# Optimization experiments

Hardware: AMD Instinct MI355X
Metric: run time of the kernel (lower is better)

Reference implementation:

```python
import jax, jax.numpy as jnp
import numpy as np

N_AGENTS = 8
STATE_DIM = 256
EMBED_DIM = 32
BATCH = 65536


def setup_inputs() -> dict:
    key = jax.random.key(0)
    ks = jax.random.split(key, 12)
    s = 1.0 / np.sqrt(STATE_DIM)
    se = 1.0 / np.sqrt(EMBED_DIM)
    return {
        "agent_qs": jax.random.normal(ks[0], (BATCH, N_AGENTS), dtype=jnp.float32),
        "states": jax.random.normal(ks[1], (BATCH, STATE_DIM), dtype=jnp.float32),
        # hyper_w_1: Linear(state_dim, embed_dim * n_agents)
        "w1_W": jax.random.uniform(ks[2], (STATE_DIM, EMBED_DIM * N_AGENTS), jnp.float32, -s, s),
        "w1_b": jax.random.uniform(ks[3], (EMBED_DIM * N_AGENTS,), jnp.float32, -s, s),
        # hyper_w_final: Linear(state_dim, embed_dim)
        "wf_W": jax.random.uniform(ks[4], (STATE_DIM, EMBED_DIM), jnp.float32, -s, s),
        "wf_b": jax.random.uniform(ks[5], (EMBED_DIM,), jnp.float32, -s, s),
        # hyper_b_1: Linear(state_dim, embed_dim)
        "b1_W": jax.random.uniform(ks[6], (STATE_DIM, EMBED_DIM), jnp.float32, -s, s),
        "b1_b": jax.random.uniform(ks[7], (EMBED_DIM,), jnp.float32, -s, s),
        # V: Linear(state_dim, embed_dim) -> ReLU -> Linear(embed_dim, 1)
        "v1_W": jax.random.uniform(ks[8], (STATE_DIM, EMBED_DIM), jnp.float32, -s, s),
        "v1_b": jax.random.uniform(ks[9], (EMBED_DIM,), jnp.float32, -s, s),
        "v2_W": jax.random.uniform(ks[10], (EMBED_DIM, 1), jnp.float32, -se, se),
        "v2_b": jax.random.uniform(ks[11], (1,), jnp.float32, -se, se),
    }


def reference(agent_qs, states, w1_W, w1_b, wf_W, wf_b, b1_W, b1_b, v1_W, v1_b, v2_W, v2_b):
    B = agent_qs.shape[0]
    # hypernet weights (abs for monotonicity)
    w1 = jnp.abs(states @ w1_W + w1_b).reshape(B, N_AGENTS, EMBED_DIM)   # [B, A, E]
    w_final = jnp.abs(states @ wf_W + wf_b)                               # [B, E]
    b1 = states @ b1_W + b1_b                                             # [B, E]
    # hidden = elu(agent_qs^T w1 + b1): [B,1,A] @ [B,A,E] -> [B,E]
    hidden = jax.nn.elu(jnp.einsum("ba,bae->be", agent_qs, w1) + b1)
    # mixed = hidden @ w_final: [B,1,E] @ [B,E,1] -> [B,1]
    mixed = jnp.sum(hidden * w_final, axis=-1, keepdims=True)             # [B, 1]
    # state value V(s)
    state_value = jax.nn.relu(states @ v1_W + v1_b) @ v2_W + v2_b         # [B, 1]
    return mixed + state_value
```

## Files before the change

### kernel.cpp

```cpp
#include <hip/hip_runtime.h>
#include <math.h>


#define NTILES 22
#define KCHUNKS 8
#define CHUNK_I4 1408

typedef __attribute__((ext_vector_type(8))) short short8;
typedef __attribute__((ext_vector_type(4))) float float4v;

__device__ __forceinline__ unsigned short f2b(float f) {
    unsigned int u = __float_as_uint(f);
    u = u + 0x7fffu + ((u >> 16) & 1u);
    return (unsigned short)(u >> 16);
}

__device__ __forceinline__ void gl2lds16(const unsigned short* g, unsigned short* l) {
    __builtin_amdgcn_global_load_lds(
        (const __attribute__((address_space(1))) unsigned int*)g,
        (__attribute__((address_space(3))) unsigned int*)l,
        16, 0, 0);
}

__global__ void repack_b(const float* __restrict__ w1_W,
                         const float* __restrict__ wf_W,
                         const float* __restrict__ b1_W,
                         const float* __restrict__ v1_W,
                         unsigned short* __restrict__ brep) {
    int idx = blockIdx.x * 256 + threadIdx.x;
    int lane = idx & 63;
    int tt   = idx >> 6;
    int t    = tt % 22;
    int kc   = tt / 22;
    int kbase = kc * 32 + (lane >> 4) * 8;
    int n = t * 16 + (lane & 15);
    short8 frag;
#pragma unroll
    for (int j = 0; j < 8; ++j) {
        int k = kbase + j;
        float val;
        if (n < 256)      val = w1_W[k * 256 + n];
        else if (n < 288) val = wf_W[k * 32 + (n - 256)];
        else if (n < 320) val = b1_W[k * 32 + (n - 288)];
        else              val = v1_W[k * 32 + (n - 320)];
        frag[j] = (short)f2b(val);
    }
    *(short8*)(&brep[idx * 8]) = frag;
}

__global__ void __launch_bounds__(256, 2)
qmix_main(const float* __restrict__ agent_qs,
          const float* __restrict__ states,
          const unsigned short* __restrict__ brep,
          const float* __restrict__ w1_b,
          const float* __restrict__ wf_b,
          const float* __restrict__ b1_b,
          const float* __restrict__ v1_b,
          const float* __restrict__ v2_W,
          const float* __restrict__ v2_b,
          float* __restrict__ out) {
    __shared__ __align__(16) unsigned short wlds[2][NTILES * 64 * 8];

    const int tid  = threadIdx.x;
    const int wave = tid >> 6, lane = tid & 63;
    const int quad = lane >> 4, l16 = lane & 15;
    const int r0 = blockIdx.x * 128 + wave * 32 + l16;
    const float* srow0 = states + (size_t)r0 * 256;
    const float* srow1 = srow0 + 16 * 256;

    for (int s = wave; s < NTILES; s += 4)
        gl2lds16(brep + (size_t)(s * 64 + lane) * 8, wlds[0] + s * 512);

    float4v s0a = *(const float4v*)(srow0 + quad * 8);
    float4v s0b = *(const float4v*)(srow0 + quad * 8 + 4);
    float4v s1a = *(const float4v*)(srow1 + quad * 8);
    float4v s1b = *(const float4v*)(srow1 + quad * 8 + 4);

    float4v acc[2][NTILES];
#pragma unroll
    for (int g = 0; g < 2; ++g)
#pragma unroll
        for (int t = 0; t < NTILES; ++t)
#pragma unroll
            for (int q = 0; q < 4; ++q) acc[g][t][q] = 0.f;

    __syncthreads();

    int cur = 0;
    for (int kc = 0; kc < KCHUNKS; ++kc) {
        if (kc < KCHUNKS - 1) {
            const unsigned short* src = brep + (size_t)(kc + 1) * CHUNK_I4 * 8;
            unsigned short* dst = wlds[cur ^ 1];
            for (int s = wave; s < NTILES; s += 4)
                gl2lds16(src + (size_t)(s * 64 + lane) * 8, dst + s * 512);
        }
        short8 b0, b1;
#pragma unroll
        for (int j = 0; j < 4; ++j) {
            b0[j] = (short)f2b(s0a[j]); b0[4 + j] = (short)f2b(s0b[j]);
            b1[j] = (short)f2b(s1a[j]); b1[4 + j] = (short)f2b(s1b[j]);
        }
        if (kc < KCHUNKS - 1) {
            const float* p0 = srow0 + (kc + 1) * 32 + quad * 8;
            const float* p1 = srow1 + (kc + 1) * 32 + quad * 8;
            s0a = *(const float4v*)(p0);
            s0b = *(const float4v*)(p0 + 4);
            s1a = *(const float4v*)(p1);
            s1b = *(const float4v*)(p1 + 4);
        }
        const short8* wb = (const short8*)wlds[cur] + lane;
#pragma unroll
        for (int t = 0; t < NTILES; ++t) {
            short8 af = wb[t * 64];
            acc[0][t] = __builtin_amdgcn_mfma_f32_16x16x32_bf16(af, b0, acc[0][t], 0, 0, 0);
            acc[1][t] = __builtin_amdgcn_mfma_f32_16x16x32_bf16(af, b1, acc[1][t], 0, 0, 0);
        }
        cur ^= 1;
        __syncthreads();
    }

#pragma unroll
    for (int g = 0; g < 2; ++g) {
        const int row = r0 + g * 16;
        float4v q0 = *(const float4v*)(agent_qs + (size_t)row * 8);
        float4v q1 = *(const float4v*)(agent_qs + (size_t)row * 8 + 4);
        float qv[8] = {q0[0], q0[1], q0[2], q0[3], q1[0], q1[1], q1[2], q1[3]};

        float qacc[8], wfv[8], b1v[8], svp = 0.f;
#pragma unroll
        for (int s = 0; s < 8; ++s) qacc[s] = 0.f;

#pragma unroll
        for (int t = 0; t < NTILES; ++t) {
            const float* bptr =
                (t < 16) ? (w1_b + t * 16) :
                (t < 18) ? (wf_b + (t - 16) * 16) :
                (t < 20) ? (b1_b + (t - 18) * 16) : (v1_b + (t - 20) * 16);
            float4v bb = *(const float4v*)(bptr + quad * 4);
            float vb[4];
#pragma unroll
            for (int j = 0; j < 4; ++j) vb[j] = acc[g][t][j] + bb[j];

            if (t < 16) {
                float q = qv[t >> 1];
                int base = (t & 1) * 4;
#pragma unroll
                for (int j = 0; j < 4; ++j) qacc[base + j] += q * fabsf(vb[j]);
            } else if (t < 18) {
                int base = (t - 16) * 4;
#pragma unroll
                for (int j = 0; j < 4; ++j) wfv[base + j] = fabsf(vb[j]);
            } else if (t < 20) {
                int base = (t - 18) * 4;
#pragma unroll
                for (int j = 0; j < 4; ++j) b1v[base + j] = vb[j];
            } else {
                int ebase = (t - 20) * 16 + quad * 4;
#pragma unroll
                for (int j = 0; j < 4; ++j)
                    svp += fmaxf(vb[j], 0.f) * v2_W[ebase + j];
            }
        }

        float mix = 0.f;
#pragma unroll
        for (int s = 0; s < 8; ++s) {
            float h = qacc[s] + b1v[s];
            h = h > 0.f ? h : (__expf(h) - 1.f);
            mix += h * wfv[s];
        }
        float tot = mix + svp;
        tot += __shfl_xor(tot, 16);
        tot += __shfl_xor(tot, 32);
        if (quad == 0) out[row] = tot + v2_b[0];
    }
}

extern "C" void kernel_launch(void* const* d_in, const int* in_sizes, int n_in,
                              void* d_out, int out_size, void* d_ws, size_t ws_size,
                              hipStream_t stream) {
    const float* agent_qs = (const float*)d_in[0];
    const float* states   = (const float*)d_in[1];
    const float* w1_W = (const float*)d_in[2];
    const float* w1_b = (const float*)d_in[3];
    const float* wf_W = (const float*)d_in[4];
    const float* wf_b = (const float*)d_in[5];
    const float* b1_W = (const float*)d_in[6];
    const float* b1_b = (const float*)d_in[7];
    const float* v1_W = (const float*)d_in[8];
    const float* v1_b = (const float*)d_in[9];
    const float* v2_W = (const float*)d_in[10];
    const float* v2_b = (const float*)d_in[11];
    float* out = (float*)d_out;
    unsigned short* brep = (unsigned short*)d_ws;

    repack_b<<<44, 256, 0, stream>>>(w1_W, wf_W, b1_W, v1_W, brep);
    qmix_main<<<512, 256, 0, stream>>>(agent_qs, states, brep,
                                       w1_b, wf_b, b1_b, v1_b, v2_W, v2_b, out);
}
```

Before: 127.2 us.

## Fuse weight repack into main kernel, converting fp32 weights to bf16 in-loop

Removes the separate repack kernel and its workspace. Each block now reads the fp32 hypernet weights directly, converts them to bf16 and writes MFMA-fragment layout into LDS, with loads and stores split around the two halves of the MFMA loop to overlap with compute. This saves one kernel launch and the workspace round trip. In exchange every one of the 512 blocks redoes the conversion, with strided scalar global loads, extra registers and more VALU work per chunk.

```diff
diff --git a/kernel.cpp b/kernel.cpp
--- a/kernel.cpp
+++ b/kernel.cpp
@@ -4,7 +4,6 @@
 
 #define NTILES 22
 #define KCHUNKS 8
-#define CHUNK_I4 1408
 
 typedef __attribute__((ext_vector_type(8))) short short8;
 typedef __attribute__((ext_vector_type(4))) float float4v;
@@ -15,50 +14,20 @@
     return (unsigned short)(u >> 16);
 }
 
-__device__ __forceinline__ void gl2lds16(const unsigned short* g, unsigned short* l) {
-    __builtin_amdgcn_global_load_lds(
-        (const __attribute__((address_space(1))) unsigned int*)g,
-        (__attribute__((address_space(3))) unsigned int*)l,
-        16, 0, 0);
-}
-
-__global__ void repack_b(const float* __restrict__ w1_W,
-                         const float* __restrict__ wf_W,
-                         const float* __restrict__ b1_W,
-                         const float* __restrict__ v1_W,
-                         unsigned short* __restrict__ brep) {
-    int idx = blockIdx.x * 256 + threadIdx.x;
-    int lane = idx & 63;
-    int tt   = idx >> 6;
-    int t    = tt % 22;
-    int kc   = tt / 22;
-    int kbase = kc * 32 + (lane >> 4) * 8;
-    int n = t * 16 + (lane & 15);
-    short8 frag;
-#pragma unroll
-    for (int j = 0; j < 8; ++j) {
-        int k = kbase + j;
-        float val;
-        if (n < 256)      val = w1_W[k * 256 + n];
-        else if (n < 288) val = wf_W[k * 32 + (n - 256)];
-        else if (n < 320) val = b1_W[k * 32 + (n - 288)];
-        else              val = v1_W[k * 32 + (n - 320)];
-        frag[j] = (short)f2b(val);
-    }
-    *(short8*)(&brep[idx * 8]) = frag;
-}
-
 __global__ void __launch_bounds__(256, 2)
-qmix_main(const float* __restrict__ agent_qs,
-          const float* __restrict__ states,
-          const unsigned short* __restrict__ brep,
-          const float* __restrict__ w1_b,
-          const float* __restrict__ wf_b,
-          const float* __restrict__ b1_b,
-          const float* __restrict__ v1_b,
-          const float* __restrict__ v2_W,
-          const float* __restrict__ v2_b,
-          float* __restrict__ out) {
+qmix_fused(const float* __restrict__ agent_qs,
+           const float* __restrict__ states,
+           const float* __restrict__ w1_W,
+           const float* __restrict__ w1_b,
+           const float* __restrict__ wf_W,
+           const float* __restrict__ wf_b,
+           const float* __restrict__ b1_W,
+           const float* __restrict__ b1_b,
+           const float* __restrict__ v1_W,
+           const float* __restrict__ v1_b,
+           const float* __restrict__ v2_W,
+           const float* __restrict__ v2_b,
+           float* __restrict__ out) {
     __shared__ __align__(16) unsigned short wlds[2][NTILES * 64 * 8];
 
     const int tid  = threadIdx.x;
@@ -68,8 +37,46 @@
     const float* srow0 = states + (size_t)r0 * 256;
     const float* srow1 = srow0 + 16 * 256;
 
-    for (int s = wave; s < NTILES; s += 4)
-        gl2lds16(brep + (size_t)(s * 64 + lane) * 8, wlds[0] + s * 512);
+#define SLOT_SRC(s_, kc_, src_, stride_) do {                            \
+        int t_ = (s_) >> 6, l_ = (s_) & 63;                              \
+        int n_ = t_ * 16 + (l_ & 15);                                    \
+        int k0_ = (kc_) * 32 + (l_ >> 4) * 8;                            \
+        if (n_ < 256)      { src_ = w1_W + (size_t)k0_ * 256 + n_;        stride_ = 256; } \
+        else if (n_ < 288) { src_ = wf_W + (size_t)k0_ * 32 + (n_ - 256); stride_ = 32;  } \
+        else if (n_ < 320) { src_ = b1_W + (size_t)k0_ * 32 + (n_ - 288); stride_ = 32;  } \
+        else               { src_ = v1_W + (size_t)k0_ * 32 + (n_ - 320); stride_ = 32;  } \
+    } while (0)
+
+#define SLOT_LOAD(rv_, s_, kc_) do {                                     \
+        const float* sp_; int st_;                                       \
+        SLOT_SRC(s_, kc_, sp_, st_);                                     \
+        _Pragma("unroll")                                                \
+        for (int j_ = 0; j_ < 8; ++j_) rv_[j_] = sp_[(size_t)j_ * st_];  \
+    } while (0)
+
+#define SLOT_STORE(rv_, s_, dst_) do {                                   \
+        short8 fr_;                                                      \
+        _Pragma("unroll")                                                \
+        for (int j_ = 0; j_ < 8; ++j_) fr_[j_] = (short)f2b(rv_[j_]);    \
+        *(short8*)((dst_) + (size_t)(s_) * 8) = fr_;                     \
+    } while (0)
+
+    {
+        unsigned short* dst = wlds[0];
+#pragma unroll
+        for (int m = 0; m < 5; ++m) {
+            int s = tid + m * 256;
+            float rv[8];
+            SLOT_LOAD(rv, s, 0);
+            SLOT_STORE(rv, s, dst);
+        }
+        if (tid < 128) {
+            int s = tid + 5 * 256;
+            float rv[8];
+            SLOT_LOAD(rv, s, 0);
+            SLOT_STORE(rv, s, dst);
+        }
+    }
 
     float4v s0a = *(const float4v*)(srow0 + quad * 8);
     float4v s0b = *(const float4v*)(srow0 + quad * 8 + 4);
@@ -86,21 +93,24 @@
 
     __syncthreads();
 
-    int cur = 0;
     for (int kc = 0; kc < KCHUNKS; ++kc) {
-        if (kc < KCHUNKS - 1) {
-            const unsigned short* src = brep + (size_t)(kc + 1) * CHUNK_I4 * 8;
-            unsigned short* dst = wlds[cur ^ 1];
-            for (int s = wave; s < NTILES; s += 4)
-                gl2lds16(src + (size_t)(s * 64 + lane) * 8, dst + s * 512);
-        }
+        const int cur = kc & 1;
+        unsigned short* nbuf = wlds[cur ^ 1];
+        const bool doconv = (kc + 1 < KCHUNKS);
+
+        float rva[3][8];
+        if (doconv) {
+#pragma unroll
+            for (int m = 0; m < 3; ++m) SLOT_LOAD(rva[m], tid + m * 256, kc + 1);
+        }
+
         short8 b0, b1;
 #pragma unroll
         for (int j = 0; j < 4; ++j) {
             b0[j] = (short)f2b(s0a[j]); b0[4 + j] = (short)f2b(s0b[j]);
             b1[j] = (short)f2b(s1a[j]); b1[4 + j] = (short)f2b(s1b[j]);
         }
-        if (kc < KCHUNKS - 1) {
+        if (doconv) {
             const float* p0 = srow0 + (kc + 1) * 32 + quad * 8;
             const float* p1 = srow1 + (kc + 1) * 32 + quad * 8;
             s0a = *(const float4v*)(p0);
@@ -108,14 +118,37 @@
             s1a = *(const float4v*)(p1);
             s1b = *(const float4v*)(p1 + 4);
         }
+
         const short8* wb = (const short8*)wlds[cur] + lane;
 #pragma unroll
-        for (int t = 0; t < NTILES; ++t) {
+        for (int t = 0; t < 11; ++t) {
             short8 af = wb[t * 64];
             acc[0][t] = __builtin_amdgcn_mfma_f32_16x16x32_bf16(af, b0, acc[0][t], 0, 0, 0);
             acc[1][t] = __builtin_amdgcn_mfma_f32_16x16x32_bf16(af, b1, acc[1][t], 0, 0, 0);
         }
-        cur ^= 1;
+
+        float rvb[3][8];
+        if (doconv) {
+#pragma unroll
+            for (int m = 0; m < 3; ++m) SLOT_STORE(rva[m], tid + m * 256, nbuf);
+            SLOT_LOAD(rvb[0], tid + 3 * 256, kc + 1);
+            SLOT_LOAD(rvb[1], tid + 4 * 256, kc + 1);
+            if (tid < 128) SLOT_LOAD(rvb[2], tid + 5 * 256, kc + 1);
+        }
+
+#pragma unroll
+        for (int t = 11; t < NTILES; ++t) {
+            short8 af = wb[t * 64];
+            acc[0][t] = __builtin_amdgcn_mfma_f32_16x16x32_bf16(af, b0, acc[0][t], 0, 0, 0);
+            acc[1][t] = __builtin_amdgcn_mfma_f32_16x16x32_bf16(af, b1, acc[1][t], 0, 0, 0);
+        }
+
+        if (doconv) {
+            SLOT_STORE(rvb[0], tid + 3 * 256, nbuf);
+            SLOT_STORE(rvb[1], tid + 4 * 256, nbuf);
+            if (tid < 128) SLOT_STORE(rvb[2], tid + 5 * 256, nbuf);
+        }
+
         __syncthreads();
     }
 
@@ -192,9 +225,9 @@
     const float* v2_W = (const float*)d_in[10];
     const float* v2_b = (const float*)d_in[11];
     float* out = (float*)d_out;
-    unsigned short* brep = (unsigned short*)d_ws;
-
-    repack_b<<<44, 256, 0, stream>>>(w1_W, wf_W, b1_W, v1_W, brep);
-    qmix_main<<<512, 256, 0, stream>>>(agent_qs, states, brep,
-                                       w1_b, wf_b, b1_b, v1_b, v2_W, v2_b, out);
+    (void)d_ws; (void)ws_size;
+
+    qmix_fused<<<512, 256, 0, stream>>>(agent_qs, states,
+                                        w1_W, w1_b, wf_W, wf_b, b1_W, b1_b,
+                                        v1_W, v1_b, v2_W, v2_b, out);
 }
```

Result: slower. 142.7 us (+12.2%).

## Fuse weight repack into main kernel with a grid-wide atomic barrier

Applied to the files above, without the earlier changes.

Drops the separate repack kernel launch. The first 44 blocks of the main kernel now do the bf16 weight repacking, and all 512 blocks then wait on a global atomic counter barrier before the GEMM phase. A memset that resets the counter is added to the stream. The aim is to save one kernel launch and its gap. The cost is a spin barrier that depends on all 512 blocks being resident at once, which needs 2 blocks per CU across 256 CUs; if they are not all resident it can deadlock.

```diff
diff --git a/kernel.cpp b/kernel.cpp
--- a/kernel.cpp
+++ b/kernel.cpp
@@ -5,6 +5,7 @@
 #define NTILES 22
 #define KCHUNKS 8
 #define CHUNK_I4 1408
+#define NBLOCKS 512
 
 typedef __attribute__((ext_vector_type(8))) short short8;
 typedef __attribute__((ext_vector_type(4))) float float4v;
@@ -22,36 +23,15 @@
         16, 0, 0);
 }
 
-__global__ void repack_b(const float* __restrict__ w1_W,
-                         const float* __restrict__ wf_W,
-                         const float* __restrict__ b1_W,
-                         const float* __restrict__ v1_W,
-                         unsigned short* __restrict__ brep) {
-    int idx = blockIdx.x * 256 + threadIdx.x;
-    int lane = idx & 63;
-    int tt   = idx >> 6;
-    int t    = tt % 22;
-    int kc   = tt / 22;
-    int kbase = kc * 32 + (lane >> 4) * 8;
-    int n = t * 16 + (lane & 15);
-    short8 frag;
-#pragma unroll
-    for (int j = 0; j < 8; ++j) {
-        int k = kbase + j;
-        float val;
-        if (n < 256)      val = w1_W[k * 256 + n];
-        else if (n < 288) val = wf_W[k * 32 + (n - 256)];
-        else if (n < 320) val = b1_W[k * 32 + (n - 288)];
-        else              val = v1_W[k * 32 + (n - 320)];
-        frag[j] = (short)f2b(val);
-    }
-    *(short8*)(&brep[idx * 8]) = frag;
-}
-
 __global__ void __launch_bounds__(256, 2)
-qmix_main(const float* __restrict__ agent_qs,
+qmix_coop(const float* __restrict__ agent_qs,
           const float* __restrict__ states,
-          const unsigned short* __restrict__ brep,
+          unsigned short* __restrict__ brep,
+          unsigned int* __restrict__ bar,
+          const float* __restrict__ w1_W,
+          const float* __restrict__ wf_W,
+          const float* __restrict__ b1_W,
+          const float* __restrict__ v1_W,
           const float* __restrict__ w1_b,
           const float* __restrict__ wf_b,
           const float* __restrict__ b1_b,
@@ -62,6 +42,42 @@
     __shared__ __align__(16) unsigned short wlds[2][NTILES * 64 * 8];
 
     const int tid  = threadIdx.x;
+
+    if (blockIdx.x < 44) {
+        int idx  = blockIdx.x * 256 + tid;
+        int lane = idx & 63;
+        int tt   = idx >> 6;
+        int t    = tt % 22;
+        int kc   = tt / 22;
+        int kbase = kc * 32 + (lane >> 4) * 8;
+        int n = t * 16 + (lane & 15);
+        short8 frag;
+#pragma unroll
+        for (int j = 0; j < 8; ++j) {
+            int k = kbase + j;
+            float val;
+            if (n < 256)      val = w1_W[k * 256 + n];
+            else if (n < 288) val = wf_W[k * 32 + (n - 256)];
+            else if (n < 320) val = b1_W[k * 32 + (n - 288)];
+            else              val = v1_W[k * 32 + (n - 320)];
+            frag[j] = (short)f2b(val);
+        }
+        *(short8*)(&brep[(size_t)idx * 8]) = frag;
+    }
+
+    __threadfence();
+    __syncthreads();
+    if (tid == 0) {
+        __hip_atomic_fetch_add(bar, 1u, __ATOMIC_ACQ_REL, __HIP_MEMORY_SCOPE_AGENT);
+        unsigned int v;
+        do {
+            v = __hip_atomic_load(bar, __ATOMIC_ACQUIRE, __HIP_MEMORY_SCOPE_AGENT);
+            if (v < NBLOCKS) __builtin_amdgcn_s_sleep(8);
+        } while (v < NBLOCKS);
+    }
+    __syncthreads();
+    __threadfence();
+
     const int wave = tid >> 6, lane = tid & 63;
     const int quad = lane >> 4, l16 = lane & 15;
     const int r0 = blockIdx.x * 128 + wave * 32 + l16;
@@ -193,8 +209,12 @@
     const float* v2_b = (const float*)d_in[11];
     float* out = (float*)d_out;
     unsigned short* brep = (unsigned short*)d_ws;
-
-    repack_b<<<44, 256, 0, stream>>>(w1_W, wf_W, b1_W, v1_W, brep);
-    qmix_main<<<512, 256, 0, stream>>>(agent_qs, states, brep,
-                                       w1_b, wf_b, b1_b, v1_b, v2_W, v2_b, out);
-}
+    unsigned int* bar = (unsigned int*)((char*)d_ws + 180224);
+
+    hipMemsetAsync((void*)bar, 0, sizeof(unsigned int), stream);
+
+    qmix_coop<<<512, 256, 0, stream>>>(agent_qs, states, brep, bar,
+                                       w1_W, wf_W, b1_W, v1_W,
+                                       w1_b, wf_b, b1_b, v1_b,
+                                       v2_W, v2_b, out);
+}
```

Measured after the change: 213.4 us. 1.68x slower.
